# Performance work log

Hardware: AMD Instinct MI355X
Metric: run time of the kernel (lower is better)

The kernel has to match this reference:

```python
import jax, jax.numpy as jnp
import numpy as np

B, S, E, H, D = 4, 2048, 1024, 8, 256  # batch, seq, embed_dim, heads, hidden_units


def setup_inputs() -> dict:
    key = jax.random.key(0)
    ks = jax.random.split(key, 9)
    scale = 0.02
    return {
        "inputA": jax.random.normal(ks[0], (B, S, E), dtype=jnp.float32),
        "WQ": jax.random.normal(ks[1], (H, E, D), dtype=jnp.float32) * scale,
        "bQ": jnp.zeros((H, D), dtype=jnp.float32),
        "WK": jax.random.normal(ks[2], (H, E, D), dtype=jnp.float32) * scale,
        "bK": jnp.zeros((H, D), dtype=jnp.float32),
        "WV": jax.random.normal(ks[3], (H, E, D), dtype=jnp.float32) * scale,
        "bV": jnp.zeros((H, D), dtype=jnp.float32),
        "WZ": jax.random.normal(ks[4], (H * D, E), dtype=jnp.float32) * scale,
        "bZ": jnp.zeros((E,), dtype=jnp.float32),
    }


def reference(inputA, WQ, bQ, WK, bK, WV, bV, WZ, bZ):
    # Per-head Linear -> ReLU (dropout=0 -> identity); heads stacked on axis h.
    Q = jax.nn.relu(jnp.einsum('bse,hed->bhsd', inputA, WQ) + bQ[None, :, None, :])
    K = jax.nn.relu(jnp.einsum('bse,hed->bhsd', inputA, WK) + bK[None, :, None, :])
    V = jax.nn.relu(jnp.einsum('bse,hed->bhsd', inputA, WV) + bV[None, :, None, :])
    # scores[b,h,s,t] ; torch bmm output was [B, S, T] per head
    scores = jnp.einsum('bhsd,bhtd->bhst', Q, K) / jnp.sqrt(jnp.float32(E))
    # double softmax: torch dim=1 (query axis s) then dim=2 (key axis t)
    A = jax.nn.softmax(scores, axis=2)
    A = jax.nn.softmax(A, axis=3)
    Z = jnp.einsum('bhst,bhtd->bhsd', A, V)
    # concat heads along feature dim (head order matches torch cat)
    Zall = Z.transpose(0, 2, 1, 3).reshape(B, S, H * D)
    return Zall @ WZ + bZ
```

## Files before the change

### kernel.cpp

```cpp
#include <hip/hip_runtime.h>

typedef __attribute__((ext_vector_type(8))) short short8;
typedef __attribute__((ext_vector_type(4))) float f32x4;

constexpr int B_ = 4, S_ = 2048, E_ = 1024, H_ = 8, D_ = 256;
constexpr int HD_ = H_ * D_;
constexpr int BS_ = B_ * S_;
constexpr int BH_ = B_ * H_;
constexpr float INV_SQRT_E = 0.03125f;

__device__ __forceinline__ unsigned short f2bf(float f) {
    union { float f; unsigned u; } x; x.f = f;
    unsigned r = (x.u + 0x7fffu + ((x.u >> 16) & 1u)) >> 16;
    return (unsigned short)r;
}

__device__ __forceinline__ void gl_lds16(const void* g, void* lds) {
    __builtin_amdgcn_global_load_lds((const __attribute__((address_space(1))) void*)g,
                                     (__attribute__((address_space(3))) void*)lds, 16, 0, 0);
}

__global__ __launch_bounds__(256) void cast_k(const float* __restrict__ src,
                                              unsigned short* __restrict__ dst, int n4) {
    int i = blockIdx.x * 256 + threadIdx.x;
    if (i >= n4) return;
    float4 v = reinterpret_cast<const float4*>(src)[i];
    ushort4 o;
    o.x = f2bf(v.x); o.y = f2bf(v.y); o.z = f2bf(v.z); o.w = f2bf(v.w);
    reinterpret_cast<ushort4*>(dst)[i] = o;
}

__global__ __launch_bounds__(256) void tcast_k(const float* __restrict__ src,
                                               unsigned short* __restrict__ dst, int R, int C) {
    __shared__ float tile[32][33];
    int b = blockIdx.z;
    const float* s = src + (size_t)b * R * C;
    unsigned short* d = dst + (size_t)b * R * C;
    int c0 = blockIdx.x * 32, r0 = blockIdx.y * 32;
    int tx = threadIdx.x, ty = threadIdx.y;
#pragma unroll
    for (int i = 0; i < 4; ++i)
        tile[ty + i * 8][tx] = s[(size_t)(r0 + ty + i * 8) * C + c0 + tx];
    __syncthreads();
#pragma unroll
    for (int i = 0; i < 4; ++i)
        d[(size_t)(c0 + ty + i * 8) * R + r0 + tx] = f2bf(tile[tx][ty + i * 8]);
}

__global__ __launch_bounds__(256) void tbf_k(const unsigned short* __restrict__ src,
                                             unsigned short* __restrict__ dst) {
    __shared__ unsigned short tile[32][33];
    int bh = blockIdx.z;
    int d0 = blockIdx.x * 32, s0 = blockIdx.y * 32;
    int tx = threadIdx.x, ty = threadIdx.y;
#pragma unroll
    for (int i = 0; i < 4; ++i)
        tile[ty + i * 8][tx] = src[((size_t)bh * S_ + s0 + ty + i * 8) * D_ + d0 + tx];
    __syncthreads();
#pragma unroll
    for (int i = 0; i < 4; ++i)
        dst[((size_t)bh * D_ + d0 + ty + i * 8) * S_ + s0 + tx] = tile[tx][ty + i * 8];
}

__global__ __launch_bounds__(256) void gemm_qkv_k(const unsigned short* __restrict__ A,
                                                  const unsigned short* __restrict__ Bt,
                                                  const float* __restrict__ bias,
                                                  unsigned short* __restrict__ out) {
    __shared__ __align__(16) unsigned short As[128 * 32];
    __shared__ __align__(16) unsigned short Bs[128 * 32];
    const int tid = threadIdx.x;
    const int wave = tid >> 6, lane = tid & 63;
    const int quad = lane >> 4, l15 = lane & 15;
    const int wm = wave >> 1, wn = wave & 1;
    const int m0 = blockIdx.y * 128, n0 = blockIdx.x * 128;
    const int c1 = tid, c2 = tid + 256;
    const int r1 = c1 >> 2, kc1 = (c1 & 3) * 8;
    const int r2 = c2 >> 2, kc2 = (c2 & 3) * 8;
    char* aB1 = (char*)As + wave * 1024; char* aB2 = aB1 + 4096;
    char* bB1 = (char*)Bs + wave * 1024; char* bB2 = bB1 + 4096;
    const unsigned short* a1 = A + (size_t)(m0 + r1) * E_ + kc1;
    const unsigned short* a2 = A + (size_t)(m0 + r2) * E_ + kc2;
    const unsigned short* b1 = Bt + (size_t)(n0 + r1) * E_ + kc1;
    const unsigned short* b2 = Bt + (size_t)(n0 + r2) * E_ + kc2;
    f32x4 acc[4][4] = {};
    for (int k0 = 0; k0 < E_; k0 += 32) {
        __syncthreads();
        gl_lds16(a1 + k0, aB1);
        gl_lds16(a2 + k0, aB2);
        gl_lds16(b1 + k0, bB1);
        gl_lds16(b2 + k0, bB2);
        __syncthreads();
        short8 af[4], bf[4];
        const short* Ass = (const short*)As;
        const short* Bss = (const short*)Bs;
#pragma unroll
        for (int f = 0; f < 4; ++f) {
            af[f] = *(const short8*)&Ass[(wm * 64 + f * 16 + l15) * 32 + quad * 8];
            bf[f] = *(const short8*)&Bss[(wn * 64 + f * 16 + l15) * 32 + quad * 8];
        }
#pragma unroll
        for (int fm = 0; fm < 4; ++fm)
#pragma unroll
            for (int fn = 0; fn < 4; ++fn)
                acc[fm][fn] = __builtin_amdgcn_mfma_f32_16x16x32_bf16(af[fm], bf[fn], acc[fm][fn], 0, 0, 0);
    }
#pragma unroll
    for (int fm = 0; fm < 4; ++fm) {
        int mbase = m0 + wm * 64 + fm * 16 + quad * 4;
#pragma unroll
        for (int fn = 0; fn < 4; ++fn) {
            int n = n0 + wn * 64 + fn * 16 + l15;
            int h = n >> 8, d = n & 255;
            float bv = bias[n];
#pragma unroll
            for (int r = 0; r < 4; ++r) {
                int m = mbase + r;
                int b = m >> 11, s = m & 2047;
                float v = fmaxf(acc[fm][fn][r] + bv, 0.0f);
                out[((size_t)(b * H_ + h) * S_ + s) * D_ + d] = f2bf(v);
            }
        }
    }
}

__global__ __launch_bounds__(256) void gemm_out_k(const unsigned short* __restrict__ A,
                                                  const unsigned short* __restrict__ Bt,
                                                  const float* __restrict__ bias,
                                                  float* __restrict__ out) {
    __shared__ __align__(16) unsigned short As[128 * 32];
    __shared__ __align__(16) unsigned short Bs[128 * 32];
    const int tid = threadIdx.x;
    const int wave = tid >> 6, lane = tid & 63;
    const int quad = lane >> 4, l15 = lane & 15;
    const int wm = wave >> 1, wn = wave & 1;
    const int m0 = blockIdx.y * 128, n0 = blockIdx.x * 128;
    const int c1 = tid, c2 = tid + 256;
    const int r1 = c1 >> 2, kc1 = (c1 & 3) * 8;
    const int r2 = c2 >> 2, kc2 = (c2 & 3) * 8;
    char* aB1 = (char*)As + wave * 1024; char* aB2 = aB1 + 4096;
    char* bB1 = (char*)Bs + wave * 1024; char* bB2 = bB1 + 4096;
    const unsigned short* a1 = A + (size_t)(m0 + r1) * HD_ + kc1;
    const unsigned short* a2 = A + (size_t)(m0 + r2) * HD_ + kc2;
    const unsigned short* b1 = Bt + (size_t)(n0 + r1) * HD_ + kc1;
    const unsigned short* b2 = Bt + (size_t)(n0 + r2) * HD_ + kc2;
    f32x4 acc[4][4] = {};
    for (int k0 = 0; k0 < HD_; k0 += 32) {
        __syncthreads();
        gl_lds16(a1 + k0, aB1);
        gl_lds16(a2 + k0, aB2);
        gl_lds16(b1 + k0, bB1);
        gl_lds16(b2 + k0, bB2);
        __syncthreads();
        short8 af[4], bf[4];
        const short* Ass = (const short*)As;
        const short* Bss = (const short*)Bs;
#pragma unroll
        for (int f = 0; f < 4; ++f) {
            af[f] = *(const short8*)&Ass[(wm * 64 + f * 16 + l15) * 32 + quad * 8];
            bf[f] = *(const short8*)&Bss[(wn * 64 + f * 16 + l15) * 32 + quad * 8];
        }
#pragma unroll
        for (int fm = 0; fm < 4; ++fm)
#pragma unroll
            for (int fn = 0; fn < 4; ++fn)
                acc[fm][fn] = __builtin_amdgcn_mfma_f32_16x16x32_bf16(af[fm], bf[fn], acc[fm][fn], 0, 0, 0);
    }
#pragma unroll
    for (int fm = 0; fm < 4; ++fm) {
        int mbase = m0 + wm * 64 + fm * 16 + quad * 4;
#pragma unroll
        for (int fn = 0; fn < 4; ++fn) {
            int n = n0 + wn * 64 + fn * 16 + l15;
            float bv = bias[n];
#pragma unroll
            for (int r = 0; r < 4; ++r)
                out[(size_t)(mbase + r) * E_ + n] = acc[fm][fn][r] + bv;
        }
    }
}

__global__ __launch_bounds__(512, 2) void colsum_k(const unsigned short* __restrict__ Q,
                                                   const unsigned short* __restrict__ K,
                                                   float* __restrict__ invLcol) {
    __shared__ float part[8][64];
    const int tid = threadIdx.x;
    const int wave = tid >> 6, lane = tid & 63;
    const int quad = lane >> 4, l15 = lane & 15;
    const int tg = wave >> 2, sg = wave & 3;
    const int bh = blockIdx.y;
    const int t0 = blockIdx.x * 128;
    const unsigned short* Qh = Q + (size_t)bh * S_ * D_;
    const unsigned short* Kh = K + (size_t)bh * S_ * D_;
    short8 kf[32];
#pragma unroll
    for (int kc = 0; kc < 8; ++kc)
#pragma unroll
        for (int fm = 0; fm < 4; ++fm)
            kf[kc * 4 + fm] = *(const short8*)&Kh[(size_t)(t0 + tg * 64 + fm * 16 + l15) * D_ + kc * 32 + quad * 8];
    float rl[4][4] = {};
    const unsigned short* Qw = Qh + (size_t)(sg * 16 + l15) * D_ + quad * 8;
    short8 qf[8];
#pragma unroll
    for (int kc = 0; kc < 8; ++kc) qf[kc] = *(const short8*)&Qw[kc * 32];
    for (int s0 = 0; s0 < S_; s0 += 64) {
        f32x4 acc[4] = {};
#pragma unroll
        for (int kc = 0; kc < 8; ++kc)
#pragma unroll
            for (int fm = 0; fm < 4; ++fm)
                acc[fm] = __builtin_amdgcn_mfma_f32_16x16x32_bf16(kf[kc * 4 + fm], qf[kc], acc[fm], 0, 0, 0);
        int sn = (s0 + 64) & (S_ - 1);
#pragma unroll
        for (int kc = 0; kc < 8; ++kc)
            qf[kc] = *(const short8*)&Qw[(size_t)sn * D_ + kc * 32];
#pragma unroll
        for (int fm = 0; fm < 4; ++fm)
#pragma unroll
            for (int r = 0; r < 4; ++r)
                rl[fm][r] += __expf(acc[fm][r] * INV_SQRT_E);
    }
#pragma unroll
    for (int fm = 0; fm < 4; ++fm)
#pragma unroll
        for (int r = 0; r < 4; ++r) {
            float v = rl[fm][r];
            v += __shfl_xor(v, 1); v += __shfl_xor(v, 2);
            v += __shfl_xor(v, 4); v += __shfl_xor(v, 8);
            if (l15 == 0) part[wave][fm * 16 + quad * 4 + r] = v;
        }
    __syncthreads();
    if (tid < 128) {
        int tg2 = tid >> 6, i = tid & 63;
        float s = part[tg2 * 4 + 0][i] + part[tg2 * 4 + 1][i] +
                  part[tg2 * 4 + 2][i] + part[tg2 * 4 + 3][i];
        invLcol[(size_t)bh * S_ + t0 + tid] = 1.0f / s;
    }
}

__global__ __launch_bounds__(512, 2) void flash8_k(const unsigned short* __restrict__ Q,
                                                   const unsigned short* __restrict__ K,
                                                   const unsigned short* __restrict__ Vt,
                                                   const float* __restrict__ invLcol,
                                                   unsigned short* __restrict__ Zall) {
    __shared__ __align__(16) unsigned short Qs[128 * 256];
    __shared__ __align__(16) unsigned short Ps[2 * 2 * 128 * 40];
    __shared__ float rsum[128];
    const int tid = threadIdx.x;
    const int wave = tid >> 6, lane = tid & 63;
    const int quad = lane >> 4, l15 = lane & 15;
    const int rg = wave >> 2, tc = wave & 3;
    const int dc = wave & 3;
    const int bh = blockIdx.y;
    const int bb = bh >> 3, hh = bh & 7;
    const int s0 = blockIdx.x * 128;
    const unsigned short* Qh = Q + (size_t)bh * S_ * D_;
    const unsigned short* Kh = K + (size_t)bh * S_ * D_;
    const unsigned short* Vh = Vt + (size_t)bh * D_ * S_;
    const float* Lc = invLcol + (size_t)bh * S_;

    {
        int row = tid >> 2, cb = (tid & 3) * 128;
        const char* src = (const char*)(Qh + (size_t)(s0 + row) * D_) + cb;
        char* dst = (char*)Qs + row * 512;
#pragma unroll
        for (int i = 0; i < 8; ++i) {
            short8 v = *(const short8*)(src + i * 16);
            int b = cb + i * 16;
            *(short8*)(dst + (b ^ ((row & 7) << 4))) = v;
        }
    }
    if (tid < 128) rsum[tid] = 0.f;
    f32x4 zacc[4][4] = {};
    float rsacc[4][4] = {};

    const char* KtBase = (const char*)(Kh + (size_t)(tc * 16 + l15) * D_ + quad * 8);
    const char* VwBase = (const char*)(Vh + (size_t)(dc * 64 + l15) * S_ + quad * 8);
    short8 kb[8], vb[8];
#pragma unroll
    for (int kc = 0; kc < 8; ++kc)
        kb[kc] = *(const short8*)(KtBase + kc * 64);
#pragma unroll
    for (int kk = 0; kk < 2; ++kk)
#pragma unroll
        for (int fn = 0; fn < 4; ++fn)
            vb[kk * 4 + fn] = *(const short8*)(VwBase + ((size_t)(fn * 16) * S_ + kk * 32) * 2);
    float Li = Lc[tc * 16 + l15];
    __syncthreads();

    for (int t0 = 0; t0 < S_; t0 += 64) {
        const int buf = (t0 >> 6) & 1;
        const int tn = (t0 + 64) & (S_ - 1);
        f32x4 acc[4] = {};
#pragma unroll
        for (int kc = 0; kc < 8; ++kc) {
            short8 qa[4];
#pragma unroll
            for (int fm = 0; fm < 4; ++fm) {
                int row = rg * 64 + fm * 16 + l15;
                int b = kc * 64 + quad * 16;
                qa[fm] = *(const short8*)((const char*)Qs + row * 512 + (b ^ ((row & 7) << 4)));
            }
#pragma unroll
            for (int fm = 0; fm < 4; ++fm)
                acc[fm] = __builtin_amdgcn_mfma_f32_16x16x32_bf16(qa[fm], kb[kc], acc[fm], 0, 0, 0);
        }
#pragma unroll
        for (int kc = 0; kc < 8; ++kc)
            kb[kc] = *(const short8*)(KtBase + (size_t)tn * D_ * 2 + kc * 64);
        float Li_n = Lc[tn + tc * 16 + l15];
        unsigned short* Pw = Ps + buf * 10240 + (tc >> 1) * 5120 + (tc & 1) * 16 + l15;
#pragma unroll
        for (int fm = 0; fm < 4; ++fm)
#pragma unroll
            for (int r = 0; r < 4; ++r) {
                float e = __expf(__expf(acc[fm][r] * INV_SQRT_E) * Li);
                rsacc[fm][r] += e;
                int row = rg * 64 + fm * 16 + quad * 4 + r;
                Pw[row * 40] = f2bf(e);
            }
        __syncthreads();
#pragma unroll
        for (int kk = 0; kk < 2; ++kk) {
            short8 pa[4];
#pragma unroll
            for (int fm = 0; fm < 4; ++fm)
                pa[fm] = *(const short8*)&Ps[buf * 10240 + kk * 5120 + (rg * 64 + fm * 16 + l15) * 40 + quad * 8];
#pragma unroll
            for (int fm = 0; fm < 4; ++fm)
#pragma unroll
                for (int fn = 0; fn < 4; ++fn)
                    zacc[fm][fn] = __builtin_amdgcn_mfma_f32_16x16x32_bf16(pa[fm], vb[kk * 4 + fn], zacc[fm][fn], 0, 0, 0);
        }
#pragma unroll
        for (int kk = 0; kk < 2; ++kk)
#pragma unroll
            for (int fn = 0; fn < 4; ++fn)
                vb[kk * 4 + fn] = *(const short8*)(VwBase + ((size_t)(fn * 16) * S_ + tn + kk * 32) * 2);
        Li = Li_n;
    }
#pragma unroll
    for (int fm = 0; fm < 4; ++fm)
#pragma unroll
        for (int r = 0; r < 4; ++r) {
            float v = rsacc[fm][r];
            v += __shfl_xor(v, 1); v += __shfl_xor(v, 2);
            v += __shfl_xor(v, 4); v += __shfl_xor(v, 8);
            if (l15 == 0) atomicAdd(&rsum[rg * 64 + fm * 16 + quad * 4 + r], v);
        }
    __syncthreads();
#pragma unroll
    for (int fm = 0; fm < 4; ++fm)
#pragma unroll
        for (int r = 0; r < 4; ++r) {
            int row = rg * 64 + fm * 16 + quad * 4 + r;
            float inv = 1.0f / rsum[row];
#pragma unroll
            for (int fn = 0; fn < 4; ++fn)
                Zall[(size_t)(bb * S_ + s0 + row) * HD_ + hh * D_ + dc * 64 + fn * 16 + l15] =
                    f2bf(zacc[fm][fn][r] * inv);
        }
}

extern "C" void kernel_launch(void* const* d_in, const int* in_sizes, int n_in,
                              void* d_out, int out_size, void* d_ws, size_t ws_size,
                              hipStream_t stream) {
    const float* Ain = (const float*)d_in[0];
    const float* WQ = (const float*)d_in[1];
    const float* bQ = (const float*)d_in[2];
    const float* WK = (const float*)d_in[3];
    const float* bK = (const float*)d_in[4];
    const float* WV = (const float*)d_in[5];
    const float* bV = (const float*)d_in[6];
    const float* WZ = (const float*)d_in[7];
    const float* bZ = (const float*)d_in[8];
    float* out = (float*)d_out;

    char* ws = (char*)d_ws;
    size_t off = 0;
    auto alloc = [&](size_t bytes) {
        char* p = ws + off;
        off += (bytes + 255) & ~(size_t)255;
        return p;
    };
    unsigned short* Abf = (unsigned short*)alloc((size_t)BS_ * E_ * 2);
    unsigned short* Wqt = (unsigned short*)alloc((size_t)H_ * D_ * E_ * 2);
    unsigned short* Wkt = (unsigned short*)alloc((size_t)H_ * D_ * E_ * 2);
    unsigned short* Wvt = (unsigned short*)alloc((size_t)H_ * D_ * E_ * 2);
    unsigned short* Wzt = (unsigned short*)alloc((size_t)E_ * HD_ * 2);
    unsigned short* Qb = (unsigned short*)alloc((size_t)BH_ * S_ * D_ * 2);
    unsigned short* Kb = (unsigned short*)alloc((size_t)BH_ * S_ * D_ * 2);
    unsigned short* Vb = (unsigned short*)alloc((size_t)BH_ * S_ * D_ * 2);
    unsigned short* Vtb = (unsigned short*)alloc((size_t)BH_ * S_ * D_ * 2);
    unsigned short* Zb = (unsigned short*)alloc((size_t)BS_ * HD_ * 2);
    float* Lc = (float*)alloc((size_t)BH_ * S_ * 4);

    dim3 tb(32, 8);
    cast_k<<<(BS_ * E_ / 4 + 255) / 256, 256, 0, stream>>>(Ain, Abf, BS_ * E_ / 4);
    tcast_k<<<dim3(D_ / 32, E_ / 32, H_), tb, 0, stream>>>(WQ, Wqt, E_, D_);
    tcast_k<<<dim3(D_ / 32, E_ / 32, H_), tb, 0, stream>>>(WK, Wkt, E_, D_);
    tcast_k<<<dim3(D_ / 32, E_ / 32, H_), tb, 0, stream>>>(WV, Wvt, E_, D_);
    tcast_k<<<dim3(E_ / 32, HD_ / 32, 1), tb, 0, stream>>>(WZ, Wzt, HD_, E_);

    gemm_qkv_k<<<dim3(HD_ / 128, BS_ / 128), 256, 0, stream>>>(Abf, Wqt, bQ, Qb);
    gemm_qkv_k<<<dim3(HD_ / 128, BS_ / 128), 256, 0, stream>>>(Abf, Wkt, bK, Kb);
    gemm_qkv_k<<<dim3(HD_ / 128, BS_ / 128), 256, 0, stream>>>(Abf, Wvt, bV, Vb);

    tbf_k<<<dim3(D_ / 32, S_ / 32, BH_), tb, 0, stream>>>(Vb, Vtb);

    colsum_k<<<dim3(S_ / 128, BH_), 512, 0, stream>>>(Qb, Kb, Lc);
    flash8_k<<<dim3(S_ / 128, BH_), 512, 0, stream>>>(Qb, Kb, Vtb, Lc, Zb);

    gemm_out_k<<<dim3(E_ / 128, BS_ / 128), 256, 0, stream>>>(Zb, Wzt, bZ, out);
}
```

Measured before the change: 724.4 us.

## Keep Q fragments in registers, stream K/V just-in-time, remap grid for XCD locality

The flash kernel now holds its Q tile as 32 register fragments per lane instead of a swizzled LDS copy, which removes LDS reads of Q from the QK inner loop and frees 64KB of shared memory. K is double-buffered two chunks at a time inside the kc loop, and V fragments are loaded per 32-column half rather than prefetched a whole tile ahead. Both colsum and flash launch a flat 1D grid whose index mapping places 8 consecutive blocks on different heads of the same sequence tile, presumably to spread heads across XCDs and improve L2 reuse. Holding Q in registers raises VGPR pressure and shortens load-latency hiding for K and V.

Result: slower. 813.3 us (+12.3%).

```diff
diff --git a/kernel.cpp b/kernel.cpp
--- a/kernel.cpp
+++ b/kernel.cpp
@@ -187,8 +187,9 @@
     const int wave = tid >> 6, lane = tid & 63;
     const int quad = lane >> 4, l15 = lane & 15;
     const int tg = wave >> 2, sg = wave & 3;
-    const int bh = blockIdx.y;
-    const int t0 = blockIdx.x * 128;
+    const int p = blockIdx.x;
+    const int bh = (p & 7) + 8 * ((p >> 3) >> 4);
+    const int t0 = ((p >> 3) & 15) * 128;
     const unsigned short* Qh = Q + (size_t)bh * S_ * D_;
     const unsigned short* Kh = K + (size_t)bh * S_ * D_;
     short8 kf[32];
@@ -237,12 +238,11 @@
     }
 }
 
-__global__ __launch_bounds__(512, 2) void flash8_k(const unsigned short* __restrict__ Q,
+__global__ __launch_bounds__(512, 2) void flash9_k(const unsigned short* __restrict__ Q,
                                                    const unsigned short* __restrict__ K,
                                                    const unsigned short* __restrict__ Vt,
                                                    const float* __restrict__ invLcol,
                                                    unsigned short* __restrict__ Zall) {
-    __shared__ __align__(16) unsigned short Qs[128 * 256];
     __shared__ __align__(16) unsigned short Ps[2 * 2 * 128 * 40];
     __shared__ float rsum[128];
     const int tid = threadIdx.x;
@@ -250,42 +250,32 @@
     const int quad = lane >> 4, l15 = lane & 15;
     const int rg = wave >> 2, tc = wave & 3;
     const int dc = wave & 3;
-    const int bh = blockIdx.y;
+    const int p = blockIdx.x;
+    const int bh = (p & 7) + 8 * ((p >> 3) >> 4);
+    const int s0 = ((p >> 3) & 15) * 128;
     const int bb = bh >> 3, hh = bh & 7;
-    const int s0 = blockIdx.x * 128;
     const unsigned short* Qh = Q + (size_t)bh * S_ * D_;
     const unsigned short* Kh = K + (size_t)bh * S_ * D_;
     const unsigned short* Vh = Vt + (size_t)bh * D_ * S_;
     const float* Lc = invLcol + (size_t)bh * S_;
 
-    {
-        int row = tid >> 2, cb = (tid & 3) * 128;
-        const char* src = (const char*)(Qh + (size_t)(s0 + row) * D_) + cb;
-        char* dst = (char*)Qs + row * 512;
-#pragma unroll
-        for (int i = 0; i < 8; ++i) {
-            short8 v = *(const short8*)(src + i * 16);
-            int b = cb + i * 16;
-            *(short8*)(dst + (b ^ ((row & 7) << 4))) = v;
-        }
-    }
+    short8 q[32];
+#pragma unroll
+    for (int kc = 0; kc < 8; ++kc)
+#pragma unroll
+        for (int fm = 0; fm < 4; ++fm)
+            q[kc * 4 + fm] = *(const short8*)&Qh[(size_t)(s0 + rg * 64 + fm * 16 + l15) * D_ + kc * 32 + quad * 8];
+
     if (tid < 128) rsum[tid] = 0.f;
     f32x4 zacc[4][4] = {};
     float rsacc[4][4] = {};
 
     const char* KtBase = (const char*)(Kh + (size_t)(tc * 16 + l15) * D_ + quad * 8);
     const char* VwBase = (const char*)(Vh + (size_t)(dc * 64 + l15) * S_ + quad * 8);
-    short8 kb[8], vb[8];
-#pragma unroll
-    for (int kc = 0; kc < 8; ++kc)
-        kb[kc] = *(const short8*)(KtBase + kc * 64);
-#pragma unroll
-    for (int kk = 0; kk < 2; ++kk)
-#pragma unroll
-        for (int fn = 0; fn < 4; ++fn)
-            vb[kk * 4 + fn] = *(const short8*)(VwBase + ((size_t)(fn * 16) * S_ + kk * 32) * 2);
     float Li = Lc[tc * 16 + l15];
-    __syncthreads();
+    short8 kb[2];
+    kb[0] = *(const short8*)(KtBase + 0 * 64);
+    kb[1] = *(const short8*)(KtBase + 1 * 64);
 
     for (int t0 = 0; t0 < S_; t0 += 64) {
         const int buf = (t0 >> 6) & 1;
@@ -293,20 +283,15 @@
         f32x4 acc[4] = {};
 #pragma unroll
         for (int kc = 0; kc < 8; ++kc) {
-            short8 qa[4];
-#pragma unroll
-            for (int fm = 0; fm < 4; ++fm) {
-                int row = rg * 64 + fm * 16 + l15;
-                int b = kc * 64 + quad * 16;
-                qa[fm] = *(const short8*)((const char*)Qs + row * 512 + (b ^ ((row & 7) << 4)));
-            }
+            short8 kbu = kb[kc & 1];
+            if (kc < 6)
+                kb[kc & 1] = *(const short8*)(KtBase + (size_t)t0 * (D_ * 2) + (kc + 2) * 64);
+            else
+                kb[kc & 1] = *(const short8*)(KtBase + (size_t)tn * (D_ * 2) + (kc - 6) * 64);
 #pragma unroll
             for (int fm = 0; fm < 4; ++fm)
-                acc[fm] = __builtin_amdgcn_mfma_f32_16x16x32_bf16(qa[fm], kb[kc], acc[fm], 0, 0, 0);
-        }
-#pragma unroll
-        for (int kc = 0; kc < 8; ++kc)
-            kb[kc] = *(const short8*)(KtBase + (size_t)tn * D_ * 2 + kc * 64);
+                acc[fm] = __builtin_amdgcn_mfma_f32_16x16x32_bf16(q[kc * 4 + fm], kbu, acc[fm], 0, 0, 0);
+        }
         float Li_n = Lc[tn + tc * 16 + l15];
         unsigned short* Pw = Ps + buf * 10240 + (tc >> 1) * 5120 + (tc & 1) * 16 + l15;
 #pragma unroll
@@ -318,24 +303,31 @@
                 int row = rg * 64 + fm * 16 + quad * 4 + r;
                 Pw[row * 40] = f2bf(e);
             }
+        short8 vb[4];
+#pragma unroll
+        for (int fn = 0; fn < 4; ++fn)
+            vb[fn] = *(const short8*)(VwBase + ((size_t)(fn * 16) * S_ + t0) * 2);
         __syncthreads();
-#pragma unroll
-        for (int kk = 0; kk < 2; ++kk) {
-            short8 pa[4];
-#pragma unroll
-            for (int fm = 0; fm < 4; ++fm)
-                pa[fm] = *(const short8*)&Ps[buf * 10240 + kk * 5120 + (rg * 64 + fm * 16 + l15) * 40 + quad * 8];
-#pragma unroll
-            for (int fm = 0; fm < 4; ++fm)
-#pragma unroll
-                for (int fn = 0; fn < 4; ++fn)
-                    zacc[fm][fn] = __builtin_amdgcn_mfma_f32_16x16x32_bf16(pa[fm], vb[kk * 4 + fn], zacc[fm][fn], 0, 0, 0);
-        }
-#pragma unroll
-        for (int kk = 0; kk < 2; ++kk)
+        short8 pa[4];
+#pragma unroll
+        for (int fm = 0; fm < 4; ++fm)
+            pa[fm] = *(const short8*)&Ps[buf * 10240 + (rg * 64 + fm * 16 + l15) * 40 + quad * 8];
+#pragma unroll
+        for (int fm = 0; fm < 4; ++fm)
 #pragma unroll
             for (int fn = 0; fn < 4; ++fn)
-                vb[kk * 4 + fn] = *(const short8*)(VwBase + ((size_t)(fn * 16) * S_ + tn + kk * 32) * 2);
+                zacc[fm][fn] = __builtin_amdgcn_mfma_f32_16x16x32_bf16(pa[fm], vb[fn], zacc[fm][fn], 0, 0, 0);
+#pragma unroll
+        for (int fn = 0; fn < 4; ++fn)
+            vb[fn] = *(const short8*)(VwBase + ((size_t)(fn * 16) * S_ + t0 + 32) * 2);
+#pragma unroll
+        for (int fm = 0; fm < 4; ++fm)
+            pa[fm] = *(const short8*)&Ps[buf * 10240 + 5120 + (rg * 64 + fm * 16 + l15) * 40 + quad * 8];
+#pragma unroll
+        for (int fm = 0; fm < 4; ++fm)
+#pragma unroll
+            for (int fn = 0; fn < 4; ++fn)
+                zacc[fm][fn] = __builtin_amdgcn_mfma_f32_16x16x32_bf16(pa[fm], vb[fn], zacc[fm][fn], 0, 0, 0);
         Li = Li_n;
     }
 #pragma unroll
@@ -407,8 +399,8 @@
 
     tbf_k<<<dim3(D_ / 32, S_ / 32, BH_), tb, 0, stream>>>(Vb, Vtb);
 
-    colsum_k<<<dim3(S_ / 128, BH_), 512, 0, stream>>>(Qb, Kb, Lc);
-    flash8_k<<<dim3(S_ / 128, BH_), 512, 0, stream>>>(Qb, Kb, Vtb, Lc, Zb);
+    colsum_k<<<dim3(BH_ * S_ / 128), 512, 0, stream>>>(Qb, Kb, Lc);
+    flash9_k<<<dim3(BH_ * S_ / 128), 512, 0, stream>>>(Qb, Kb, Vtb, Lc, Zb);
 
     gemm_out_k<<<dim3(E_ / 128, BS_ / 128), 256, 0, stream>>>(Zb, Wzt, bZ, out);
 }
```
